# Kernel tuning notes

Measured on AMD Instinct MI355X. Metric: run time of the kernel, lower is better.

The kernel has to match this reference:

```python
import jax, jax.numpy as jnp
import numpy as np

N_ROUTINGS = 3


def squash(v, axis=-1):
    sn = jnp.sum(jnp.square(v), axis=axis, keepdims=True)
    return (jnp.sqrt(sn) / (1.0 + sn)) * v


def setup_inputs() -> dict:
    key = jax.random.key(0)
    k1, k2 = jax.random.split(key)
    B, R, C, n_in, d_in = 16, 14, 14, 64, 16
    n_caps, caps_dim = 10, 16
    inputs = jax.random.normal(k1, (B, R, C, n_in, d_in), dtype=jnp.float32)
    W = jax.random.normal(k2, (n_caps, n_in, d_in, caps_dim), dtype=jnp.float32) * 0.1
    return {"inputs": inputs, "W": W}


def reference(inputs, W):
    # inputs: [B,R,C,i,e], W: [n,i,e,o] -> res (u_hat): [B,R,C,n,i,o]
    res = jnp.einsum('brcie,nieo->brcnio', inputs, W)
    n_in = inputs.shape[3]
    # softmax of zeros over last axis -> uniform 1/n_in
    b = jnp.full(res.shape[:-1], 1.0 / n_in, dtype=res.dtype)  # [B,R,C,n,i]
    for _ in range(N_ROUTINGS - 1):
        v = squash(jnp.sum(b[..., None] * res, axis=-2))  # [B,R,C,n,o]
        b = b + jnp.sum(res * v[..., None, :], axis=-1)   # agreement
    out = squash(jnp.sum(b[..., None] * res, axis=-2))
    return out  # [B,R,C,n_caps,caps_dim]
```

## Files before the change

### kernel.cpp

```cpp
#include <hip/hip_runtime.h>
#include <hip/hip_bf16.h>

typedef __attribute__((ext_vector_type(4))) float f32x4;
typedef __attribute__((ext_vector_type(8))) short s16x8;
typedef __attribute__((ext_vector_type(2))) __fp16 h16x2;


template<int CTRL>
__device__ __forceinline__ float dpp_add(float x) {
    int v = __builtin_amdgcn_update_dpp(0, __float_as_int(x), CTRL, 0xF, 0xF, true);
    return x + __int_as_float(v);
}
template<int CTRL>
__device__ __forceinline__ int dpp_mov(int x) {
    return __builtin_amdgcn_update_dpp(0, x, CTRL, 0xF, 0xF, true);
}
__device__ __forceinline__ h16x2 bch(int x) { return __builtin_bit_cast(h16x2, x); }
__device__ __forceinline__ int bci(h16x2 x) { return __builtin_bit_cast(int, x); }

__global__ __launch_bounds__(256, 4) void caps_kernel(
    const float* __restrict__ inp,
    const float* __restrict__ W,
    float* __restrict__ out)
{
    const int tid = threadIdx.x;
    const int w   = tid >> 6;
    const int l   = tid & 63;
    const int n   = blockIdx.x / 196;
    const int pg  = blockIdx.x % 196;
    const int pos0 = pg * 16;

    extern __shared__ __align__(16) char smem[];
    char* rbuf = smem;

    const int i4 = l >> 2;
    const int oq = l & 3;
    const int i_ = w * 16 + i4;
    const int col = l & 15;
    const int kg  = l >> 4;

    const float* wb = W + (size_t)n * 16384 + i_ * 256 + oq * 4;
    h16x2 wpk[32];
#pragma unroll
    for (int r = 0; r < 4; ++r) {
        int c = (oq + r) & 3;
        f32x4 w0 = *(const f32x4*)(wb + (c * 4 + 0) * 16);
        f32x4 w1 = *(const f32x4*)(wb + (c * 4 + 1) * 16);
        f32x4 w2 = *(const f32x4*)(wb + (c * 4 + 2) * 16);
        f32x4 w3 = *(const f32x4*)(wb + (c * 4 + 3) * 16);
#pragma unroll
        for (int dd = 0; dd < 4; ++dd) {
            wpk[r * 8 + dd]     = __builtin_amdgcn_cvt_pkrtz(w0[dd], w1[dd]);
            wpk[r * 8 + 4 + dd] = __builtin_amdgcn_cvt_pkrtz(w2[dd], w3[dd]);
        }
    }

    f32x4 raw[16];
#pragma unroll
    for (int pp = 0; pp < 16; ++pp)
        raw[pp] = *(const f32x4*)(inp + (size_t)(pos0 + pp) * 1024 + w * 256 + l * 4);

    s16x8 ones;
#pragma unroll
    for (int j = 0; j < 8; ++j) ones[j] = (short)0x3F80;

#pragma unroll
    for (int pp = 0; pp < 16; ++pp) {
        f32x4 a = raw[pp];
        int iA = bci(__builtin_amdgcn_cvt_pkrtz(a[0], a[1]));
        int iB = bci(__builtin_amdgcn_cvt_pkrtz(a[2], a[3]));
        float acc0 = 0.f, acc1 = 0.f, acc2 = 0.f, acc3 = 0.f;

        acc0 = __builtin_amdgcn_fdot2(bch(iA), wpk[0], acc0, false);
        acc1 = __builtin_amdgcn_fdot2(bch(iA), wpk[1], acc1, false);
        acc2 = __builtin_amdgcn_fdot2(bch(iA), wpk[2], acc2, false);
        acc3 = __builtin_amdgcn_fdot2(bch(iA), wpk[3], acc3, false);
        acc0 = __builtin_amdgcn_fdot2(bch(iB), wpk[4], acc0, false);
        acc1 = __builtin_amdgcn_fdot2(bch(iB), wpk[5], acc1, false);
        acc2 = __builtin_amdgcn_fdot2(bch(iB), wpk[6], acc2, false);
        acc3 = __builtin_amdgcn_fdot2(bch(iB), wpk[7], acc3, false);
        {
            int jA = dpp_mov<0x39>(iA), jB = dpp_mov<0x39>(iB);
            acc0 = __builtin_amdgcn_fdot2(bch(jA), wpk[8],  acc0, false);
            acc1 = __builtin_amdgcn_fdot2(bch(jA), wpk[9],  acc1, false);
            acc2 = __builtin_amdgcn_fdot2(bch(jA), wpk[10], acc2, false);
            acc3 = __builtin_amdgcn_fdot2(bch(jA), wpk[11], acc3, false);
            acc0 = __builtin_amdgcn_fdot2(bch(jB), wpk[12], acc0, false);
            acc1 = __builtin_amdgcn_fdot2(bch(jB), wpk[13], acc1, false);
            acc2 = __builtin_amdgcn_fdot2(bch(jB), wpk[14], acc2, false);
            acc3 = __builtin_amdgcn_fdot2(bch(jB), wpk[15], acc3, false);
        }
        {
            int jA = dpp_mov<0x4E>(iA), jB = dpp_mov<0x4E>(iB);
            acc0 = __builtin_amdgcn_fdot2(bch(jA), wpk[16], acc0, false);
            acc1 = __builtin_amdgcn_fdot2(bch(jA), wpk[17], acc1, false);
            acc2 = __builtin_amdgcn_fdot2(bch(jA), wpk[18], acc2, false);
            acc3 = __builtin_amdgcn_fdot2(bch(jA), wpk[19], acc3, false);
            acc0 = __builtin_amdgcn_fdot2(bch(jB), wpk[20], acc0, false);
            acc1 = __builtin_amdgcn_fdot2(bch(jB), wpk[21], acc1, false);
            acc2 = __builtin_amdgcn_fdot2(bch(jB), wpk[22], acc2, false);
            acc3 = __builtin_amdgcn_fdot2(bch(jB), wpk[23], acc3, false);
        }
        {
            int jA = dpp_mov<0x93>(iA), jB = dpp_mov<0x93>(iB);
            acc0 = __builtin_amdgcn_fdot2(bch(jA), wpk[24], acc0, false);
            acc1 = __builtin_amdgcn_fdot2(bch(jA), wpk[25], acc1, false);
            acc2 = __builtin_amdgcn_fdot2(bch(jA), wpk[26], acc2, false);
            acc3 = __builtin_amdgcn_fdot2(bch(jA), wpk[27], acc3, false);
            acc0 = __builtin_amdgcn_fdot2(bch(jB), wpk[28], acc0, false);
            acc1 = __builtin_amdgcn_fdot2(bch(jB), wpk[29], acc1, false);
            acc2 = __builtin_amdgcn_fdot2(bch(jB), wpk[30], acc2, false);
            acc3 = __builtin_amdgcn_fdot2(bch(jB), wpk[31], acc3, false);
        }

        float accv[4] = {acc0, acc1, acc2, acc3};
#pragma unroll
        for (int dd = 0; dd < 4; ++dd) {
            int o = oq * 4 + dd;
            __hip_bfloat16 bb = __float2bfloat16(accv[dd]);
            int byte = pp * 2048 + o * 128 + (((i_ >> 3) ^ (o & 7)) << 4) + (i_ & 7) * 2;
            *(unsigned short*)(rbuf + byte) = *(unsigned short*)&bb;
        }
    }

    asm volatile("s_waitcnt lgkmcnt(0)" ::: "memory");
    __builtin_amdgcn_s_barrier();
    asm volatile("" ::: "memory");
    __builtin_amdgcn_sched_barrier(0);

    float s[4];
    f32x4 G[4];
#pragma unroll
    for (int c = 0; c < 4; ++c) {
        const int pp = c * 4 + w;
        s16x8 fr0 = *(const s16x8*)(rbuf + pp * 2048 + col * 128 + (((kg + 0) ^ (col & 7)) << 4));
        s16x8 fr1 = *(const s16x8*)(rbuf + pp * 2048 + col * 128 + (((kg + 4) ^ (col & 7)) << 4));
        f32x4 g  = (f32x4)0.0f;
        f32x4 c2 = (f32x4)0.0f;
        g  = __builtin_amdgcn_mfma_f32_16x16x32_bf16(fr0, fr0, g, 0, 0, 0);
        g  = __builtin_amdgcn_mfma_f32_16x16x32_bf16(fr1, fr1, g, 0, 0, 0);
        c2 = __builtin_amdgcn_mfma_f32_16x16x32_bf16(ones, fr0, c2, 0, 0, 0);
        c2 = __builtin_amdgcn_mfma_f32_16x16x32_bf16(ones, fr1, c2, 0, 0, 0);
        G[c] = g;
        s[c] = c2[0] * (1.0f / 64.0f);
    }

#pragma unroll
    for (int it = 0; it < 2; ++it) {
#pragma unroll
        for (int c = 0; c < 4; ++c) {
            float sn = s[c] * s[c];
            sn = dpp_add<0xB1>(sn);
            sn = dpp_add<0x4E>(sn);
            sn = dpp_add<0x124>(sn);
            sn = dpp_add<0x128>(sn);
            float scale = sqrtf(sn) / (1.0f + sn);
            float v = scale * s[c];
            float v0 = __shfl(v, kg * 4 + 0);
            float v1 = __shfl(v, kg * 4 + 1);
            float v2 = __shfl(v, kg * 4 + 2);
            float v3 = __shfl(v, kg * 4 + 3);
            float acc = G[c][0] * v0 + G[c][1] * v1 + G[c][2] * v2 + G[c][3] * v3;
            acc += __shfl_xor(acc, 16);
            acc += __shfl_xor(acc, 32);
            s[c] += acc;
        }
    }

#pragma unroll
    for (int c = 0; c < 4; ++c) {
        float sn = s[c] * s[c];
        sn = dpp_add<0xB1>(sn);
        sn = dpp_add<0x4E>(sn);
        sn = dpp_add<0x124>(sn);
        sn = dpp_add<0x128>(sn);
        float scale = sqrtf(sn) / (1.0f + sn);
        float v = scale * s[c];
        if (l < 16)
            out[((size_t)(pos0 + c * 4 + w) * 10 + n) * 16 + col] = v;
    }
}

extern "C" void kernel_launch(void* const* d_in, const int* in_sizes, int n_in,
                              void* d_out, int out_size, void* d_ws, size_t ws_size,
                              hipStream_t stream) {
    const float* inp = (const float*)d_in[0];
    const float* W   = (const float*)d_in[1];
    float* out = (float*)d_out;

    dim3 grid(1960), block(256);
    hipLaunchKernelGGL(caps_kernel, grid, block, 32768, stream, inp, W, out);
}
```

Before: 32.85 us.

## Give each wavefront an independent position-quad and capsule to drop block barrier

Work is repartitioned so each wavefront owns 4 positions for a single output capsule. It loops over all 64 input capsules in four groups, reloading W for each group, and writes into a private 8KB LDS slice, so the block-wide barrier goes away. Block indices are also swizzled across 8 groups, likely for XCD-aware locality. The cost is reloading and converting W four times per wave and far less reuse of input loads across capsules, in exchange for removing the block barrier.

```diff
diff --git a/kernel.cpp b/kernel.cpp
--- a/kernel.cpp
+++ b/kernel.cpp
@@ -26,115 +26,114 @@
     const int tid = threadIdx.x;
     const int w   = tid >> 6;
     const int l   = tid & 63;
-    const int n   = blockIdx.x / 196;
-    const int pg  = blockIdx.x % 196;
-    const int pos0 = pg * 16;
+
+    const int bid  = blockIdx.x;
+    const int widx = (bid & 7) * 245 + (bid >> 3);
+    const int u    = widx * 4 + w;
+    const int quad = u / 10;
+    const int n    = u - quad * 10;
 
     extern __shared__ __align__(16) char smem[];
-    char* rbuf = smem;
+    char* rbuf = smem + w * 8192;
 
     const int i4 = l >> 2;
     const int oq = l & 3;
-    const int i_ = w * 16 + i4;
     const int col = l & 15;
     const int kg  = l >> 4;
-
-    const float* wb = W + (size_t)n * 16384 + i_ * 256 + oq * 4;
-    h16x2 wpk[32];
-#pragma unroll
-    for (int r = 0; r < 4; ++r) {
-        int c = (oq + r) & 3;
-        f32x4 w0 = *(const f32x4*)(wb + (c * 4 + 0) * 16);
-        f32x4 w1 = *(const f32x4*)(wb + (c * 4 + 1) * 16);
-        f32x4 w2 = *(const f32x4*)(wb + (c * 4 + 2) * 16);
-        f32x4 w3 = *(const f32x4*)(wb + (c * 4 + 3) * 16);
-#pragma unroll
-        for (int dd = 0; dd < 4; ++dd) {
-            wpk[r * 8 + dd]     = __builtin_amdgcn_cvt_pkrtz(w0[dd], w1[dd]);
-            wpk[r * 8 + 4 + dd] = __builtin_amdgcn_cvt_pkrtz(w2[dd], w3[dd]);
-        }
-    }
-
-    f32x4 raw[16];
-#pragma unroll
-    for (int pp = 0; pp < 16; ++pp)
-        raw[pp] = *(const f32x4*)(inp + (size_t)(pos0 + pp) * 1024 + w * 256 + l * 4);
 
     s16x8 ones;
 #pragma unroll
     for (int j = 0; j < 8; ++j) ones[j] = (short)0x3F80;
 
 #pragma unroll
-    for (int pp = 0; pp < 16; ++pp) {
-        f32x4 a = raw[pp];
-        int iA = bci(__builtin_amdgcn_cvt_pkrtz(a[0], a[1]));
-        int iB = bci(__builtin_amdgcn_cvt_pkrtz(a[2], a[3]));
-        float acc0 = 0.f, acc1 = 0.f, acc2 = 0.f, acc3 = 0.f;
+    for (int sg = 0; sg < 4; ++sg) {
+        const int irow = sg * 16 + i4;
 
-        acc0 = __builtin_amdgcn_fdot2(bch(iA), wpk[0], acc0, false);
-        acc1 = __builtin_amdgcn_fdot2(bch(iA), wpk[1], acc1, false);
-        acc2 = __builtin_amdgcn_fdot2(bch(iA), wpk[2], acc2, false);
-        acc3 = __builtin_amdgcn_fdot2(bch(iA), wpk[3], acc3, false);
-        acc0 = __builtin_amdgcn_fdot2(bch(iB), wpk[4], acc0, false);
-        acc1 = __builtin_amdgcn_fdot2(bch(iB), wpk[5], acc1, false);
-        acc2 = __builtin_amdgcn_fdot2(bch(iB), wpk[6], acc2, false);
-        acc3 = __builtin_amdgcn_fdot2(bch(iB), wpk[7], acc3, false);
-        {
-            int jA = dpp_mov<0x39>(iA), jB = dpp_mov<0x39>(iB);
-            acc0 = __builtin_amdgcn_fdot2(bch(jA), wpk[8],  acc0, false);
-            acc1 = __builtin_amdgcn_fdot2(bch(jA), wpk[9],  acc1, false);
-            acc2 = __builtin_amdgcn_fdot2(bch(jA), wpk[10], acc2, false);
-            acc3 = __builtin_amdgcn_fdot2(bch(jA), wpk[11], acc3, false);
-            acc0 = __builtin_amdgcn_fdot2(bch(jB), wpk[12], acc0, false);
-            acc1 = __builtin_amdgcn_fdot2(bch(jB), wpk[13], acc1, false);
-            acc2 = __builtin_amdgcn_fdot2(bch(jB), wpk[14], acc2, false);
-            acc3 = __builtin_amdgcn_fdot2(bch(jB), wpk[15], acc3, false);
-        }
-        {
-            int jA = dpp_mov<0x4E>(iA), jB = dpp_mov<0x4E>(iB);
-            acc0 = __builtin_amdgcn_fdot2(bch(jA), wpk[16], acc0, false);
-            acc1 = __builtin_amdgcn_fdot2(bch(jA), wpk[17], acc1, false);
-            acc2 = __builtin_amdgcn_fdot2(bch(jA), wpk[18], acc2, false);
-            acc3 = __builtin_amdgcn_fdot2(bch(jA), wpk[19], acc3, false);
-            acc0 = __builtin_amdgcn_fdot2(bch(jB), wpk[20], acc0, false);
-            acc1 = __builtin_amdgcn_fdot2(bch(jB), wpk[21], acc1, false);
-            acc2 = __builtin_amdgcn_fdot2(bch(jB), wpk[22], acc2, false);
-            acc3 = __builtin_amdgcn_fdot2(bch(jB), wpk[23], acc3, false);
-        }
-        {
-            int jA = dpp_mov<0x93>(iA), jB = dpp_mov<0x93>(iB);
-            acc0 = __builtin_amdgcn_fdot2(bch(jA), wpk[24], acc0, false);
-            acc1 = __builtin_amdgcn_fdot2(bch(jA), wpk[25], acc1, false);
-            acc2 = __builtin_amdgcn_fdot2(bch(jA), wpk[26], acc2, false);
-            acc3 = __builtin_amdgcn_fdot2(bch(jA), wpk[27], acc3, false);
-            acc0 = __builtin_amdgcn_fdot2(bch(jB), wpk[28], acc0, false);
-            acc1 = __builtin_amdgcn_fdot2(bch(jB), wpk[29], acc1, false);
-            acc2 = __builtin_amdgcn_fdot2(bch(jB), wpk[30], acc2, false);
-            acc3 = __builtin_amdgcn_fdot2(bch(jB), wpk[31], acc3, false);
+        const float* wb = W + (size_t)n * 16384 + irow * 256 + oq * 4;
+        h16x2 wpk[32];
+#pragma unroll
+        for (int r = 0; r < 4; ++r) {
+            int c = (oq + r) & 3;
+            f32x4 w0 = *(const f32x4*)(wb + (c * 4 + 0) * 16);
+            f32x4 w1 = *(const f32x4*)(wb + (c * 4 + 1) * 16);
+            f32x4 w2 = *(const f32x4*)(wb + (c * 4 + 2) * 16);
+            f32x4 w3 = *(const f32x4*)(wb + (c * 4 + 3) * 16);
+#pragma unroll
+            for (int dd = 0; dd < 4; ++dd) {
+                wpk[r * 8 + dd]     = __builtin_amdgcn_cvt_pkrtz(w0[dd], w1[dd]);
+                wpk[r * 8 + 4 + dd] = __builtin_amdgcn_cvt_pkrtz(w2[dd], w3[dd]);
+            }
         }
 
-        float accv[4] = {acc0, acc1, acc2, acc3};
 #pragma unroll
-        for (int dd = 0; dd < 4; ++dd) {
-            int o = oq * 4 + dd;
-            __hip_bfloat16 bb = __float2bfloat16(accv[dd]);
-            int byte = pp * 2048 + o * 128 + (((i_ >> 3) ^ (o & 7)) << 4) + (i_ & 7) * 2;
-            *(unsigned short*)(rbuf + byte) = *(unsigned short*)&bb;
+        for (int p = 0; p < 4; ++p) {
+            f32x4 a = *(const f32x4*)(inp + (size_t)quad * 4096 + p * 1024 + irow * 16 + oq * 4);
+            int iA = bci(__builtin_amdgcn_cvt_pkrtz(a[0], a[1]));
+            int iB = bci(__builtin_amdgcn_cvt_pkrtz(a[2], a[3]));
+            float acc0 = 0.f, acc1 = 0.f, acc2 = 0.f, acc3 = 0.f;
+
+            acc0 = __builtin_amdgcn_fdot2(bch(iA), wpk[0], acc0, false);
+            acc1 = __builtin_amdgcn_fdot2(bch(iA), wpk[1], acc1, false);
+            acc2 = __builtin_amdgcn_fdot2(bch(iA), wpk[2], acc2, false);
+            acc3 = __builtin_amdgcn_fdot2(bch(iA), wpk[3], acc3, false);
+            acc0 = __builtin_amdgcn_fdot2(bch(iB), wpk[4], acc0, false);
+            acc1 = __builtin_amdgcn_fdot2(bch(iB), wpk[5], acc1, false);
+            acc2 = __builtin_amdgcn_fdot2(bch(iB), wpk[6], acc2, false);
+            acc3 = __builtin_amdgcn_fdot2(bch(iB), wpk[7], acc3, false);
+            {
+                int jA = dpp_mov<0x39>(iA), jB = dpp_mov<0x39>(iB);
+                acc0 = __builtin_amdgcn_fdot2(bch(jA), wpk[8],  acc0, false);
+                acc1 = __builtin_amdgcn_fdot2(bch(jA), wpk[9],  acc1, false);
+                acc2 = __builtin_amdgcn_fdot2(bch(jA), wpk[10], acc2, false);
+                acc3 = __builtin_amdgcn_fdot2(bch(jA), wpk[11], acc3, false);
+                acc0 = __builtin_amdgcn_fdot2(bch(jB), wpk[12], acc0, false);
+                acc1 = __builtin_amdgcn_fdot2(bch(jB), wpk[13], acc1, false);
+                acc2 = __builtin_amdgcn_fdot2(bch(jB), wpk[14], acc2, false);
+                acc3 = __builtin_amdgcn_fdot2(bch(jB), wpk[15], acc3, false);
+            }
+            {
+                int jA = dpp_mov<0x4E>(iA), jB = dpp_mov<0x4E>(iB);
+                acc0 = __builtin_amdgcn_fdot2(bch(jA), wpk[16], acc0, false);
+                acc1 = __builtin_amdgcn_fdot2(bch(jA), wpk[17], acc1, false);
+                acc2 = __builtin_amdgcn_fdot2(bch(jA), wpk[18], acc2, false);
+                acc3 = __builtin_amdgcn_fdot2(bch(jA), wpk[19], acc3, false);
+                acc0 = __builtin_amdgcn_fdot2(bch(jB), wpk[20], acc0, false);
+                acc1 = __builtin_amdgcn_fdot2(bch(jB), wpk[21], acc1, false);
+                acc2 = __builtin_amdgcn_fdot2(bch(jB), wpk[22], acc2, false);
+                acc3 = __builtin_amdgcn_fdot2(bch(jB), wpk[23], acc3, false);
+            }
+            {
+                int jA = dpp_mov<0x93>(iA), jB = dpp_mov<0x93>(iB);
+                acc0 = __builtin_amdgcn_fdot2(bch(jA), wpk[24], acc0, false);
+                acc1 = __builtin_amdgcn_fdot2(bch(jA), wpk[25], acc1, false);
+                acc2 = __builtin_amdgcn_fdot2(bch(jA), wpk[26], acc2, false);
+                acc3 = __builtin_amdgcn_fdot2(bch(jA), wpk[27], acc3, false);
+                acc0 = __builtin_amdgcn_fdot2(bch(jB), wpk[28], acc0, false);
+                acc1 = __builtin_amdgcn_fdot2(bch(jB), wpk[29], acc1, false);
+                acc2 = __builtin_amdgcn_fdot2(bch(jB), wpk[30], acc2, false);
+                acc3 = __builtin_amdgcn_fdot2(bch(jB), wpk[31], acc3, false);
+            }
+
+            float accv[4] = {acc0, acc1, acc2, acc3};
+#pragma unroll
+            for (int dd = 0; dd < 4; ++dd) {
+                int o = oq * 4 + dd;
+                __hip_bfloat16 bb = __float2bfloat16(accv[dd]);
+                int byte = p * 2048 + o * 128 + (((irow >> 3) ^ (o & 7)) << 4) + (irow & 7) * 2;
+                *(unsigned short*)(rbuf + byte) = *(unsigned short*)&bb;
+            }
         }
     }
 
     asm volatile("s_waitcnt lgkmcnt(0)" ::: "memory");
-    __builtin_amdgcn_s_barrier();
-    asm volatile("" ::: "memory");
     __builtin_amdgcn_sched_barrier(0);
 
     float s[4];
     f32x4 G[4];
 #pragma unroll
     for (int c = 0; c < 4; ++c) {
-        const int pp = c * 4 + w;
-        s16x8 fr0 = *(const s16x8*)(rbuf + pp * 2048 + col * 128 + (((kg + 0) ^ (col & 7)) << 4));
-        s16x8 fr1 = *(const s16x8*)(rbuf + pp * 2048 + col * 128 + (((kg + 4) ^ (col & 7)) << 4));
+        s16x8 fr0 = *(const s16x8*)(rbuf + c * 2048 + col * 128 + (((kg + 0) ^ (col & 7)) << 4));
+        s16x8 fr1 = *(const s16x8*)(rbuf + c * 2048 + col * 128 + (((kg + 4) ^ (col & 7)) << 4));
         f32x4 g  = (f32x4)0.0f;
         f32x4 c2 = (f32x4)0.0f;
         g  = __builtin_amdgcn_mfma_f32_16x16x32_bf16(fr0, fr0, g, 0, 0, 0);
@@ -177,7 +176,7 @@
         float scale = sqrtf(sn) / (1.0f + sn);
         float v = scale * s[c];
         if (l < 16)
-            out[((size_t)(pos0 + c * 4 + w) * 10 + n) * 16 + col] = v;
+            out[((size_t)(quad * 4 + c) * 10 + n) * 16 + col] = v;
     }
 }
 
```

Result: slower. 74.64 us (+127.3%).
